# Kernel tuning notes

Measured on AMD Instinct MI355X. Metric: run time of the kernel, lower is better.

## Reference

```python
import jax, jax.numpy as jnp
import numpy as np

S, B, D, H = 2048, 2, 256, 8
DK = D // H
EPS = 1e-6
NEG = -1.0e9


def setup_inputs() -> dict:
    key = jax.random.key(0)
    ks = jax.random.split(key, 10)
    s = 1.0 / np.sqrt(D)
    return {
        "q": jax.random.normal(ks[0], (S, B, D), jnp.float32),
        "k": jax.random.normal(ks[1], (S, B, D), jnp.float32),
        "v": jax.random.normal(ks[2], (S, B, D), jnp.float32),
        "graph_pos": jax.random.uniform(ks[3], (S, S, H), jnp.float32),
        "mask": jax.random.randint(ks[4], (B, S, S), 0, 2, jnp.int32),
        # linear weights stored [in, out] so y = x @ W (torch Linear W.T)
        "w_q": jax.random.normal(ks[5], (D, D), jnp.float32) * s,
        "w_k": jax.random.normal(ks[6], (D, D), jnp.float32) * s,
        "w_v": jax.random.normal(ks[7], (D, D), jnp.float32) * s,
        "w_fc": jax.random.normal(ks[8], (D, D), jnp.float32) * s,
        "ln_gamma": jnp.ones((D,), jnp.float32),
        "ln_beta": jnp.zeros((D,), jnp.float32),
    }


def _forward(q, k, v, graph_pos, mask, w_q, w_k, w_v, w_fc, ln_gamma, ln_beta):
    # seq-first -> batch-first: [B, S, D]
    qb = jnp.transpose(q, (1, 0, 2))
    kb = jnp.transpose(k, (1, 0, 2))
    vb = jnp.transpose(v, (1, 0, 2))
    residual = qb
    # project and split heads: [B, H, S, dk]
    qh = (qb @ w_q).reshape(B, S, H, DK).transpose(0, 2, 1, 3)
    kh = (kb @ w_k).reshape(B, S, H, DK).transpose(0, 2, 1, 3)
    vh = (vb @ w_v).reshape(B, S, H, DK).transpose(0, 2, 1, 3)
    temp = jnp.asarray(DK, jnp.float32) ** 0.5
    attn = jnp.einsum("bhqd,bhkd->bhqk", qh / temp, kh)
    attn = jnp.where(mask[:, None] == 0, NEG, attn)
    attno = jax.nn.softmax(attn, axis=-1)  # dropout is identity in eval
    # graph_pos [lk, lq, h] -> [1, h, lq, lk], multiply post-softmax
    bias = jnp.transpose(graph_pos, (2, 1, 0))[None]
    out = jnp.einsum("bhqk,bhkd->bhqd", attno * bias, vh)
    out = out.transpose(0, 2, 1, 3).reshape(B, S, D)
    out = out @ w_fc + residual
    mu = out.mean(-1, keepdims=True)
    var = out.var(-1, keepdims=True)
    out = (out - mu) * jax.lax.rsqrt(var + EPS) * ln_gamma + ln_beta
    return jnp.transpose(out, (1, 0, 2)), attno


def reference(q, k, v, graph_pos, mask, w_q, w_k, w_v, w_fc, ln_gamma, ln_beta):
    return _forward(q, k, v, graph_pos, mask, w_q, w_k, w_v, w_fc, ln_gamma, ln_beta)
```

## Files before the change

### kernel.cpp

```cpp
#include <hip/hip_runtime.h>
#include <hip/hip_bf16.h>

#define S_LEN 2048
#define BATCH 2
#define DMODEL 256
#define NHEAD 8
#define DKH 32
#define NTOK (S_LEN * BATCH)
#define OUT0_ELEMS ((size_t)NTOK * DMODEL)
#define SW (S_LEN / 32)

typedef __bf16 bf16_t;
typedef __bf16 bf16x8 __attribute__((ext_vector_type(8)));
typedef __bf16 bf16x4 __attribute__((ext_vector_type(4)));
typedef float f32x4 __attribute__((ext_vector_type(4)));

#define MFMA16(a, b, c) __builtin_amdgcn_mfma_f32_16x16x32_bf16(a, b, c, 0, 0, 0)

__global__ void k_probe(const unsigned short* __restrict__ q, int* __restrict__ flag) {
  if (threadIdx.x == 0 && blockIdx.x == 0) {
    int good = 0;
    for (int i = 0; i < 512; i += 2) {
      unsigned short u = q[i];
      int e = (u >> 7) & 0xFF;
      if ((u & 0x7FFF) == 0 || (e >= 110 && e <= 135)) good++;
    }
    *flag = (good >= 200) ? 0 : 1;
  }
}

__global__ __launch_bounds__(256) void k_convert3(
    const void* __restrict__ s0, const void* __restrict__ s1,
    const void* __restrict__ s2, bf16_t* __restrict__ d0,
    bf16_t* __restrict__ d1, bf16_t* __restrict__ d2, int n,
    const int* __restrict__ flag) {
  const void* src = (blockIdx.y == 0) ? s0 : (blockIdx.y == 1) ? s1 : s2;
  bf16_t* dst = (blockIdx.y == 0) ? d0 : (blockIdx.y == 1) ? d1 : d2;
  int i = blockIdx.x * 256 + threadIdx.x;
  if (i >= n) return;
  if (*flag) dst[i] = (bf16_t)((const float*)src)[i];
  else       dst[i] = ((const bf16_t*)src)[i];
}

__global__ __launch_bounds__(256) void k_transpose_w(
    const void* __restrict__ w_q, const void* __restrict__ w_k,
    const void* __restrict__ w_v, const void* __restrict__ w_fc,
    bf16_t* __restrict__ wt, const int* __restrict__ flag) {
  __shared__ bf16_t tile[32][33];
  const void* w = (blockIdx.z == 0) ? w_q : (blockIdx.z == 1) ? w_k
                                       : (blockIdx.z == 2) ? w_v : w_fc;
  int f = *flag;
  bf16_t* o = wt + (size_t)blockIdx.z * DMODEL * DMODEL;
  int tx = threadIdx.x, ty = threadIdx.y;
  int x = blockIdx.x * 32 + tx;
  int y0 = blockIdx.y * 32;
  for (int j = ty; j < 32; j += 8) {
    size_t idx = (size_t)(y0 + j) * DMODEL + x;
    float v = f ? ((const float*)w)[idx] : (float)((const bf16_t*)w)[idx];
    tile[j][tx] = (bf16_t)v;
  }
  __syncthreads();
  for (int j = ty; j < 32; j += 8)
    o[(size_t)(blockIdx.x * 32 + j) * DMODEL + y0 + tx] = tile[tx][j];
}

__global__ __launch_bounds__(256) void k_proj(
    const bf16_t* __restrict__ qin, const bf16_t* __restrict__ kin,
    const bf16_t* __restrict__ vin, const bf16_t* __restrict__ wt,
    bf16_t* __restrict__ qhi, bf16_t* __restrict__ qlo,
    bf16_t* __restrict__ khi, bf16_t* __restrict__ klo,
    bf16_t* __restrict__ vt) {
  int mat = blockIdx.z;
  const bf16_t* x = (mat == 0) ? qin : (mat == 1) ? kin : vin;
  const bf16_t* wm = wt + (size_t)mat * DMODEL * DMODEL;
  int t0 = blockIdx.x * 16;
  int lane = threadIdx.x & 63, wave = threadIdx.x >> 6;
  int col = lane & 15, quad = lane >> 4;
  f32x4 acc[4] = {};
  const bf16_t* xrow = x + (size_t)(t0 + col) * DMODEL + quad * 8;
  for (int kk = 0; kk < 8; kk++) {
    bf16x8 a = *(const bf16x8*)(xrow + kk * 32);
#pragma unroll
    for (int nt = 0; nt < 4; nt++) {
      int n0 = wave * 64 + nt * 16;
      bf16x8 bw = *(const bf16x8*)(wm + (size_t)(n0 + col) * DMODEL + kk * 32 + quad * 8);
      acc[nt] = MFMA16(a, bw, acc[nt]);
    }
  }
  const float qscale = 0.17677669529663687f;
#pragma unroll
  for (int nt = 0; nt < 4; nt++) {
    int n = wave * 64 + nt * 16 + col;
    int h = n >> 5, dk = n & 31;
#pragma unroll
    for (int r = 0; r < 4; r++) {
      int t = t0 + quad * 4 + r;
      int s = t >> 1, bb = t & 1;
      float val = acc[nt][r];
      if (mat == 0) val *= qscale;
      if (mat <= 1) {
        bf16_t hi = (bf16_t)val;
        bf16_t lo = (bf16_t)(val - (float)hi);
        size_t idx = ((size_t)(bb * NHEAD + h) * S_LEN + s) * DKH + dk;
        if (mat == 0) { qhi[idx] = hi; qlo[idx] = lo; }
        else         { khi[idx] = hi; klo[idx] = lo; }
      } else {
        vt[((size_t)(bb * NHEAD + h) * DKH + dk) * S_LEN + s] = (bf16_t)val;
      }
    }
  }
}

template <int MODE>
__global__ __launch_bounds__(256) void k_tr_gp(
    const void* __restrict__ gp, bf16_t* __restrict__ gpt,
    void* __restrict__ attno_raw, const int* __restrict__ mask,
    unsigned int* __restrict__ mbits, const int* __restrict__ flag) {
  __shared__ float tile[32][8][32];
  int is32 = *flag;
  int tid = threadIdx.x;
  int k0 = blockIdx.x * 32, q0 = blockIdx.y * 32;
  int ci = tid & 63, krl = tid >> 6;
#pragma unroll
  for (int p = 0; p < 8; p++) {
    int kr = p * 4 + krl;
    size_t base = ((size_t)(k0 + kr) * S_LEN + q0) * NHEAD + ci * 4;
    f32x4 v;
    if (is32) {
      v = __builtin_nontemporal_load((const f32x4*)((const float*)gp + base));
    } else {
      bf16x4 bv = *(const bf16x4*)((const bf16_t*)gp + base);
      v[0] = (float)bv[0]; v[1] = (float)bv[1];
      v[2] = (float)bv[2]; v[3] = (float)bv[3];
    }
    int qq = ci >> 1, hb = (ci & 1) * 4;
    tile[kr][hb + 0][qq] = v[0];
    tile[kr][hb + 1][qq] = v[1];
    tile[kr][hb + 2][qq] = v[2];
    tile[kr][hb + 3][qq] = v[3];
  }
  __syncthreads();
  int h = tid >> 5, q = tid & 31;
  if (MODE == 0) {
    bf16_t* orow = gpt + ((size_t)h * S_LEN + q0 + q) * S_LEN + k0;
#pragma unroll
    for (int j = 0; j < 4; j++) {
      bf16x8 o;
#pragma unroll
      for (int i2 = 0; i2 < 8; i2++) o[i2] = (bf16_t)tile[j * 8 + i2][h][q];
      *(bf16x8*)(orow + j * 8) = o;
    }
  } else {
    size_t ro = ((size_t)h * S_LEN + q0 + q) * S_LEN + k0;
    size_t bs = (size_t)NHEAD * S_LEN * S_LEN;
    if (is32) {
      float* o0 = (float*)attno_raw + OUT0_ELEMS + ro;
#pragma unroll
      for (int j = 0; j < 8; j++) {
        f32x4 o;
#pragma unroll
        for (int i2 = 0; i2 < 4; i2++) o[i2] = tile[j * 4 + i2][h][q];
        *(f32x4*)(o0 + j * 4) = o;
        *(f32x4*)(o0 + bs + j * 4) = o;
      }
    } else {
      bf16_t* o0 = (bf16_t*)attno_raw + OUT0_ELEMS + ro;
#pragma unroll
      for (int j = 0; j < 4; j++) {
        bf16x8 o;
#pragma unroll
        for (int i2 = 0; i2 < 8; i2++) o[i2] = (bf16_t)tile[j * 8 + i2][h][q];
        *(bf16x8*)(o0 + j * 8) = o;
        *(bf16x8*)(o0 + bs + j * 8) = o;
      }
    }
  }
  if (tid < 64) {
    int w = (blockIdx.y * 64 + blockIdx.x) * 64 + tid;
    const int* src = mask + (size_t)w * 32;
    unsigned int bits = 0;
#pragma unroll
    for (int j = 0; j < 32; j += 4) {
      int4 m = *(const int4*)(src + j);
      if (m.x) bits |= 1u << j;
      if (m.y) bits |= 1u << (j + 1);
      if (m.z) bits |= 1u << (j + 2);
      if (m.w) bits |= 1u << (j + 3);
    }
    mbits[w] = bits;
  }
}

template <int BMODE>
__global__ __launch_bounds__(256) void k_attn(
    const bf16_t* __restrict__ qhi, const bf16_t* __restrict__ qlo,
    const bf16_t* __restrict__ khi, const bf16_t* __restrict__ klo,
    const bf16_t* __restrict__ vtg, const bf16_t* __restrict__ gpt,
    const unsigned int* __restrict__ mbits, void* __restrict__ attno_raw,
    float* __restrict__ attn_out, const int* __restrict__ flag) {
  __shared__ __align__(16) bf16_t lds_p[4][16][72];
  __shared__ __align__(16) bf16_t lds_pb[4][16][72];
  __shared__ float lds_m[4][16];
  __shared__ float lds_l[4][16];

  int is32 = *flag;
  float*  attno_f = (float*)attno_raw + OUT0_ELEMS;
  bf16_t* attno_b = (bf16_t*)attno_raw + OUT0_ELEMS;

  int L = blockIdx.x;
  int j = L >> 3;
  int p = (L & 7) + ((j >> 7) << 3);
  int h = p >> 1, b = p & 1;
  int q0 = (j & 127) * 16;

  int lane = threadIdx.x & 63, wave = threadIdx.x >> 6;
  int col = lane & 15, quad = lane >> 4;
  int kbase = wave * 512;
  size_t head = (size_t)(b * NHEAD + h);
  const bf16_t* Qh = qhi + head * S_LEN * DKH;
  const bf16_t* Ql = qlo + head * S_LEN * DKH;
  const bf16_t* Kh = khi + head * S_LEN * DKH;
  const bf16_t* Kl = klo + head * S_LEN * DKH;
  const bf16_t* Vt = vtg + head * DKH * S_LEN;
  const unsigned int* mrow =
      mbits + ((size_t)b * S_LEN + q0 + col) * SW + (kbase >> 5);
  const bf16_t* gprow = gpt + ((size_t)h * S_LEN + q0 + col) * S_LEN + kbase;
  size_t brow = head * S_LEN * S_LEN + (size_t)(q0 + col) * S_LEN + kbase;

  bf16x8 qhF = *(const bf16x8*)(Qh + (q0 + col) * DKH + quad * 8);
  bf16x8 qlF = *(const bf16x8*)(Ql + (q0 + col) * DKH + quad * 8);

  float m = -3.0e38f, l = 0.f;
#pragma unroll
  for (int t = 0; t < 32; t++) {
    int k0 = kbase + t * 16;
    bf16x8 khF = *(const bf16x8*)(Kh + (size_t)(k0 + col) * DKH + quad * 8);
    bf16x8 klF = *(const bf16x8*)(Kl + (size_t)(k0 + col) * DKH + quad * 8);
    f32x4 sc = {};
    sc = MFMA16(khF, qhF, sc);
    sc = MFMA16(khF, qlF, sc);
    sc = MFMA16(klF, qhF, sc);
    unsigned int mw = mrow[t >> 1];
    int mb = (int)(mw >> ((t & 1) * 16 + quad * 4)) & 0xF;
    float s0 = (mb & 1) ? sc[0] : -1e9f;
    float s1 = (mb & 2) ? sc[1] : -1e9f;
    float s2 = (mb & 4) ? sc[2] : -1e9f;
    float s3 = (mb & 8) ? sc[3] : -1e9f;
    float tm = fmaxf(fmaxf(s0, s1), fmaxf(s2, s3));
    float m2 = fmaxf(m, tm);
    l = l * __expf(m - m2) + __expf(s0 - m2) + __expf(s1 - m2) +
        __expf(s2 - m2) + __expf(s3 - m2);
    m = m2;
  }
#pragma unroll
  for (int off = 16; off < 64; off <<= 1) {
    float mo = __shfl_xor(m, off);
    float lo2 = __shfl_xor(l, off);
    float mn = fmaxf(m, mo);
    l = l * __expf(m - mn) + lo2 * __expf(mo - mn);
    m = mn;
  }
  if (lane < 16) { lds_m[wave][lane] = m; lds_l[wave][lane] = l; }
  __syncthreads();
  {
    float mg = -3.0e38f;
#pragma unroll
    for (int w = 0; w < 4; w++) mg = fmaxf(mg, lds_m[w][col]);
    float lg = 0.f;
#pragma unroll
    for (int w = 0; w < 4; w++) lg += lds_l[w][col] * __expf(lds_m[w][col] - mg);
    m = mg;
    l = lg;
  }
  float invl = 1.0f / l;

  f32x4 oacc[2] = {};
  for (int c = 0; c < 8; c++) {
#pragma unroll
    for (int tt = 0; tt < 4; tt++) {
      int k0 = kbase + c * 64 + tt * 16;
      bf16x8 khF = *(const bf16x8*)(Kh + (size_t)(k0 + col) * DKH + quad * 8);
      bf16x8 klF = *(const bf16x8*)(Kl + (size_t)(k0 + col) * DKH + quad * 8);
      f32x4 sc = {};
      sc = MFMA16(khF, qhF, sc);
      sc = MFMA16(khF, qlF, sc);
      sc = MFMA16(klF, qhF, sc);
      unsigned int mw = mrow[c * 2 + (tt >> 1)];
      int mb = (int)(mw >> ((tt & 1) * 16 + quad * 4)) & 0xF;
      float bias[4];
      if (BMODE == 0) {
        bf16x4 b4 = *(const bf16x4*)(gprow + c * 64 + tt * 16 + quad * 4);
#pragma unroll
        for (int r = 0; r < 4; r++) bias[r] = (float)b4[r];
      } else {
        if (is32) {
          f32x4 b4 = *(const f32x4*)(attno_f + brow + c * 64 + tt * 16 + quad * 4);
#pragma unroll
          for (int r = 0; r < 4; r++) bias[r] = b4[r];
        } else {
          bf16x4 b4 = *(const bf16x4*)(attno_b + brow + c * 64 + tt * 16 + quad * 4);
#pragma unroll
          for (int r = 0; r < 4; r++) bias[r] = (float)b4[r];
        }
      }
      bf16x4 pv, pbv;
#pragma unroll
      for (int r = 0; r < 4; r++) {
        float sv = (mb & (1 << r)) ? sc[r] : -1e9f;
        float p = __expf(sv - m) * invl;
        pv[r] = (bf16_t)p;
        pbv[r] = (bf16_t)(p * bias[r]);
      }
      *(bf16x4*)&lds_p[wave][col][tt * 16 + quad * 4] = pv;
      *(bf16x4*)&lds_pb[wave][col][tt * 16 + quad * 4] = pbv;
    }
    {
      int r = lane >> 2, part = lane & 3;
      size_t base = head * S_LEN * S_LEN + (size_t)(q0 + r) * S_LEN + kbase + c * 64 + part * 16;
      if (is32) {
#pragma unroll
        for (int jj = 0; jj < 4; jj++) {
          f32x4 vv;
#pragma unroll
          for (int ii = 0; ii < 4; ii++)
            vv[ii] = (float)lds_p[wave][r][part * 16 + jj * 4 + ii];
          *(f32x4*)(attno_f + base + jj * 4) = vv;
        }
      } else {
        bf16x8 v0 = *(const bf16x8*)&lds_p[wave][r][part * 16];
        bf16x8 v1 = *(const bf16x8*)&lds_p[wave][r][part * 16 + 8];
        *(bf16x8*)(attno_b + base) = v0;
        *(bf16x8*)(attno_b + base + 8) = v1;
      }
    }
#pragma unroll
    for (int ks = 0; ks < 2; ks++) {
      bf16x8 pf = *(const bf16x8*)&lds_pb[wave][col][ks * 32 + quad * 8];
#pragma unroll
      for (int dt = 0; dt < 2; dt++) {
        bf16x8 vf = *(const bf16x8*)(Vt + (size_t)(dt * 16 + col) * S_LEN + kbase + c * 64 + ks * 32 + quad * 8);
        oacc[dt] = MFMA16(vf, pf, oacc[dt]);
      }
    }
  }
  {
    float* lo = (float*)&lds_p[wave][0][0];
#pragma unroll
    for (int dt = 0; dt < 2; dt++)
#pragma unroll
      for (int r = 0; r < 4; r++)
        lo[col * 34 + dt * 16 + quad * 4 + r] = oacc[dt][r];
  }
  __syncthreads();
  if (wave == 0) {
    int t = (q0 + col) * BATCH + b;
#pragma unroll
    for (int dt = 0; dt < 2; dt++) {
      f32x4 vv = {};
#pragma unroll
      for (int w = 0; w < 4; w++) {
        const float* lw = (const float*)&lds_p[w][0][0];
#pragma unroll
        for (int r2 = 0; r2 < 4; r2++)
          vv[r2] += lw[col * 34 + dt * 16 + quad * 4 + r2];
      }
      *(f32x4*)(attn_out + (size_t)t * DMODEL + h * DKH + dt * 16 + quad * 4) = vv;
    }
  }
}

__global__ __launch_bounds__(256) void k_fc_ln(
    const float* __restrict__ attn_out, const bf16_t* __restrict__ wtfc,
    const bf16_t* __restrict__ qc, const void* __restrict__ gamma,
    const void* __restrict__ beta, void* __restrict__ out0,
    const int* __restrict__ flag) {
  __shared__ float lds_sx[4][16];
  __shared__ float lds_sq[4][16];
  int is32 = *flag;
  int t0 = blockIdx.x * 16;
  int lane = threadIdx.x & 63, wave = threadIdx.x >> 6;
  int col = lane & 15, quad = lane >> 4;
  f32x4 acc[4] = {};
  const float* arow = attn_out + (size_t)(t0 + col) * DMODEL + quad * 8;
  for (int kk = 0; kk < 8; kk++) {
    float4 a0 = *(const float4*)(arow + kk * 32);
    float4 a1 = *(const float4*)(arow + kk * 32 + 4);
    float av[8] = {a0.x, a0.y, a0.z, a0.w, a1.x, a1.y, a1.z, a1.w};
    bf16x8 ahi, alo;
#pragma unroll
    for (int j = 0; j < 8; j++) {
      bf16_t hi = (bf16_t)av[j];
      ahi[j] = hi;
      alo[j] = (bf16_t)(av[j] - (float)hi);
    }
#pragma unroll
    for (int nt = 0; nt < 4; nt++) {
      int n0 = wave * 64 + nt * 16;
      bf16x8 bfr = *(const bf16x8*)(wtfc + (size_t)(n0 + col) * DMODEL + kk * 32 + quad * 8);
      acc[nt] = MFMA16(ahi, bfr, acc[nt]);
      acc[nt] = MFMA16(alo, bfr, acc[nt]);
    }
  }
#pragma unroll
  for (int nt = 0; nt < 4; nt++) {
    int n = wave * 64 + nt * 16 + col;
#pragma unroll
    for (int r = 0; r < 4; r++) {
      int t = t0 + quad * 4 + r;
      acc[nt][r] += (float)qc[(size_t)t * DMODEL + n];
    }
  }
  float sx[4], sq[4];
#pragma unroll
  for (int r = 0; r < 4; r++) {
    float s = 0, s2 = 0;
#pragma unroll
    for (int nt = 0; nt < 4; nt++) { float v = acc[nt][r]; s += v; s2 += v * v; }
    sx[r] = s; sq[r] = s2;
  }
#pragma unroll
  for (int off = 1; off < 16; off <<= 1) {
#pragma unroll
    for (int r = 0; r < 4; r++) {
      sx[r] += __shfl_xor(sx[r], off);
      sq[r] += __shfl_xor(sq[r], off);
    }
  }
  if (col == 0) {
#pragma unroll
    for (int r = 0; r < 4; r++) {
      lds_sx[wave][quad * 4 + r] = sx[r];
      lds_sq[wave][quad * 4 + r] = sq[r];
    }
  }
  __syncthreads();
#pragma unroll
  for (int r = 0; r < 4; r++) {
    int tl = quad * 4 + r;
    float tsx = lds_sx[0][tl] + lds_sx[1][tl] + lds_sx[2][tl] + lds_sx[3][tl];
    float tsq = lds_sq[0][tl] + lds_sq[1][tl] + lds_sq[2][tl] + lds_sq[3][tl];
    float mu = tsx * (1.0f / 256.0f);
    float var = tsq * (1.0f / 256.0f) - mu * mu;
    float rs = rsqrtf(var + 1e-6f);
    int t = t0 + tl;
#pragma unroll
    for (int nt = 0; nt < 4; nt++) {
      int n = wave * 64 + nt * 16 + col;
      float g = is32 ? ((const float*)gamma)[n] : (float)((const bf16_t*)gamma)[n];
      float bt = is32 ? ((const float*)beta)[n] : (float)((const bf16_t*)beta)[n];
      float val = (acc[nt][r] - mu) * rs * g + bt;
      if (is32) ((float*)out0)[(size_t)t * DMODEL + n] = val;
      else      ((bf16_t*)out0)[(size_t)t * DMODEL + n] = (bf16_t)val;
    }
  }
}

extern "C" void kernel_launch(void* const* d_in, const int* in_sizes, int n_in,
                              void* d_out, int out_size, void* d_ws, size_t ws_size,
                              hipStream_t stream) {
  (void)in_sizes; (void)n_in; (void)out_size;
  const void* qin   = d_in[0];
  const void* kin   = d_in[1];
  const void* vin   = d_in[2];
  const void* gp    = d_in[3];
  const int*  mask  = (const int*)d_in[4];
  const void* w_q   = d_in[5];
  const void* w_k   = d_in[6];
  const void* w_v   = d_in[7];
  const void* w_fc  = d_in[8];
  const void* gamma = d_in[9];
  const void* beta  = d_in[10];

  char* ws = (char*)d_ws;
  bf16_t* wt  = (bf16_t*)(ws);
  bf16_t* qc  = (bf16_t*)(ws + (1u << 20));
  bf16_t* kc  = (bf16_t*)(ws + (3u << 20));
  bf16_t* vc  = (bf16_t*)(ws + (5u << 20));
  bf16_t* qhi = (bf16_t*)(ws + (7u << 20));
  bf16_t* qlo = (bf16_t*)(ws + (9u << 20));
  bf16_t* khi = (bf16_t*)(ws + (11u << 20));
  bf16_t* klo = (bf16_t*)(ws + (13u << 20));
  bf16_t* vt  = (bf16_t*)(ws + (15u << 20));
  float* attn_out = (float*)(ws + (17u << 20));
  int* flag = (int*)(ws + (21u << 20));
  unsigned int* mbits = (unsigned int*)(ws + (3u << 20));
  bf16_t* gpt = (bf16_t*)(ws + (22u << 20));

  bool use_ws_gpt = ws_size >= (((size_t)86 << 20) + 64);

  const int NELEM_QKV = NTOK * DMODEL;

  hipLaunchKernelGGL(k_probe, dim3(1), dim3(64), 0, stream,
                     (const unsigned short*)qin, flag);
  hipLaunchKernelGGL(k_convert3, dim3((NELEM_QKV + 255) / 256, 3), dim3(256), 0, stream,
                     qin, kin, vin, qc, kc, vc, NELEM_QKV, flag);
  hipLaunchKernelGGL(k_transpose_w, dim3(8, 8, 4), dim3(32, 8), 0, stream,
                     w_q, w_k, w_v, w_fc, wt, flag);
  hipLaunchKernelGGL(k_proj, dim3(256, 1, 3), dim3(256), 0, stream,
                     qc, kc, vc, wt, qhi, qlo, khi, klo, vt);
  if (use_ws_gpt) {
    hipLaunchKernelGGL((k_tr_gp<0>), dim3(64, 64), dim3(256), 0, stream,
                       gp, gpt, d_out, mask, mbits, flag);
    hipLaunchKernelGGL((k_attn<0>), dim3(2048), dim3(256), 0, stream,
                       qhi, qlo, khi, klo, vt, gpt, mbits, d_out, attn_out, flag);
  } else {
    hipLaunchKernelGGL((k_tr_gp<1>), dim3(64, 64), dim3(256), 0, stream,
                       gp, gpt, d_out, mask, mbits, flag);
    hipLaunchKernelGGL((k_attn<1>), dim3(2048), dim3(256), 0, stream,
                       qhi, qlo, khi, klo, vt, gpt, mbits, d_out, attn_out, flag);
  }
  hipLaunchKernelGGL(k_fc_ln, dim3(256), dim3(256), 0, stream,
                     attn_out, wt + 3 * DMODEL * DMODEL, qc, gamma, beta, d_out, flag);
}
```

Baseline: 626.7 us.

## Merge prep kernels, use exp2 softmax, write attention probs directly, tune occupancy

Three preprocessing kernels (input conversion, weight transpose, graph_pos transpose with mask packing) become one launch, and the probe kernel now uses a wave-parallel reduction. The softmax switches to hardware exp2, with log2(e) folded into the q scale, so each exponential needs no extra multiply. Attention probabilities are written straight from registers to global memory, which removes the lds_p staging buffer and cuts LDS use. k_attn gets an occupancy hint, and the graph bias loads are nontemporal. Per-thread stores of the probability output are narrower and less coalesced than the old staged writes, which may cost write bandwidth.

```diff
diff --git a/kernel.cpp b/kernel.cpp
--- a/kernel.cpp
+++ b/kernel.cpp
@@ -17,51 +17,145 @@
 
 #define MFMA16(a, b, c) __builtin_amdgcn_mfma_f32_16x16x32_bf16(a, b, c, 0, 0, 0)
 
+#if defined(__has_builtin)
+#if __has_builtin(__builtin_amdgcn_exp2f)
+#define EXP2(x) __builtin_amdgcn_exp2f(x)
+#endif
+#endif
+#ifndef EXP2
+#define EXP2(x) __expf((x) * 0.6931471805599453f)
+#endif
+
 __global__ void k_probe(const unsigned short* __restrict__ q, int* __restrict__ flag) {
-  if (threadIdx.x == 0 && blockIdx.x == 0) {
-    int good = 0;
-    for (int i = 0; i < 512; i += 2) {
-      unsigned short u = q[i];
-      int e = (u >> 7) & 0xFF;
-      if ((u & 0x7FFF) == 0 || (e >= 110 && e <= 135)) good++;
-    }
-    *flag = (good >= 200) ? 0 : 1;
-  }
+  int lane = threadIdx.x & 63;
+  int good = 0;
+#pragma unroll
+  for (int j = 0; j < 4; j++) {
+    unsigned short u = q[(lane * 4 + j) * 2];
+    int e = (u >> 7) & 0xFF;
+    if ((u & 0x7FFF) == 0 || (e >= 110 && e <= 135)) good++;
+  }
+#pragma unroll
+  for (int off = 1; off < 64; off <<= 1) good += __shfl_xor(good, off);
+  if (threadIdx.x == 0) *flag = (good >= 200) ? 0 : 1;
 }
 
-__global__ __launch_bounds__(256) void k_convert3(
-    const void* __restrict__ s0, const void* __restrict__ s1,
-    const void* __restrict__ s2, bf16_t* __restrict__ d0,
-    bf16_t* __restrict__ d1, bf16_t* __restrict__ d2, int n,
-    const int* __restrict__ flag) {
-  const void* src = (blockIdx.y == 0) ? s0 : (blockIdx.y == 1) ? s1 : s2;
-  bf16_t* dst = (blockIdx.y == 0) ? d0 : (blockIdx.y == 1) ? d1 : d2;
-  int i = blockIdx.x * 256 + threadIdx.x;
-  if (i >= n) return;
-  if (*flag) dst[i] = (bf16_t)((const float*)src)[i];
-  else       dst[i] = ((const bf16_t*)src)[i];
-}
-
-__global__ __launch_bounds__(256) void k_transpose_w(
+__global__ __launch_bounds__(256) void k_prep(
+    const void* __restrict__ qin, const void* __restrict__ kin,
+    const void* __restrict__ vin, bf16_t* __restrict__ qc,
+    bf16_t* __restrict__ kc, bf16_t* __restrict__ vc,
     const void* __restrict__ w_q, const void* __restrict__ w_k,
     const void* __restrict__ w_v, const void* __restrict__ w_fc,
-    bf16_t* __restrict__ wt, const int* __restrict__ flag) {
-  __shared__ bf16_t tile[32][33];
-  const void* w = (blockIdx.z == 0) ? w_q : (blockIdx.z == 1) ? w_k
-                                       : (blockIdx.z == 2) ? w_v : w_fc;
-  int f = *flag;
-  bf16_t* o = wt + (size_t)blockIdx.z * DMODEL * DMODEL;
-  int tx = threadIdx.x, ty = threadIdx.y;
-  int x = blockIdx.x * 32 + tx;
-  int y0 = blockIdx.y * 32;
-  for (int j = ty; j < 32; j += 8) {
-    size_t idx = (size_t)(y0 + j) * DMODEL + x;
-    float v = f ? ((const float*)w)[idx] : (float)((const bf16_t*)w)[idx];
-    tile[j][tx] = (bf16_t)v;
+    bf16_t* __restrict__ wt, const void* __restrict__ gp,
+    bf16_t* __restrict__ gpt, void* __restrict__ attno_raw,
+    const int* __restrict__ mask, unsigned int* __restrict__ mbits,
+    const int* __restrict__ flag, int mode) {
+  __shared__ __align__(16) char smem[32768];
+  int bid = blockIdx.x, tid = threadIdx.x;
+  int is32 = *flag;
+
+  if (bid < 12288) {
+    int which = bid >> 12;
+    int i = (bid & 4095) * 256 + tid;
+    const void* src = (which == 0) ? qin : (which == 1) ? kin : vin;
+    bf16_t* dst = (which == 0) ? qc : (which == 1) ? kc : vc;
+    if (i < NTOK * DMODEL)
+      dst[i] = is32 ? (bf16_t)((const float*)src)[i] : ((const bf16_t*)src)[i];
+    return;
+  }
+
+  if (bid < 12544) {
+    auto tile = (bf16_t(*)[33])smem;
+    int b2 = bid - 12288;
+    int bz = b2 >> 6, bx = b2 & 7, by = (b2 >> 3) & 7;
+    const void* w = (bz == 0) ? w_q : (bz == 1) ? w_k : (bz == 2) ? w_v : w_fc;
+    bf16_t* o = wt + (size_t)bz * DMODEL * DMODEL;
+    int tx = tid & 31, ty = tid >> 5;
+    int x = bx * 32 + tx, y0 = by * 32;
+    for (int j = ty; j < 32; j += 8) {
+      size_t idx = (size_t)(y0 + j) * DMODEL + x;
+      float v = is32 ? ((const float*)w)[idx] : (float)((const bf16_t*)w)[idx];
+      tile[j][tx] = (bf16_t)v;
+    }
+    __syncthreads();
+    for (int j = ty; j < 32; j += 8)
+      o[(size_t)(bx * 32 + j) * DMODEL + y0 + tx] = tile[tx][j];
+    return;
+  }
+
+  auto tile = (float(*)[8][32])smem;
+  int b3 = bid - 12544;
+  int bx = b3 & 63, by = b3 >> 6;
+  int k0 = bx * 32, q0 = by * 32;
+  int ci = tid & 63, krl = tid >> 6;
+#pragma unroll
+  for (int p = 0; p < 8; p++) {
+    int kr = p * 4 + krl;
+    size_t base = ((size_t)(k0 + kr) * S_LEN + q0) * NHEAD + ci * 4;
+    f32x4 v;
+    if (is32) {
+      v = __builtin_nontemporal_load((const f32x4*)((const float*)gp + base));
+    } else {
+      bf16x4 bv = *(const bf16x4*)((const bf16_t*)gp + base);
+      v[0] = (float)bv[0]; v[1] = (float)bv[1];
+      v[2] = (float)bv[2]; v[3] = (float)bv[3];
+    }
+    int qq = ci >> 1, hb = (ci & 1) * 4;
+    tile[kr][hb + 0][qq] = v[0];
+    tile[kr][hb + 1][qq] = v[1];
+    tile[kr][hb + 2][qq] = v[2];
+    tile[kr][hb + 3][qq] = v[3];
   }
   __syncthreads();
-  for (int j = ty; j < 32; j += 8)
-    o[(size_t)(blockIdx.x * 32 + j) * DMODEL + y0 + tx] = tile[tx][j];
+  int h = tid >> 5, q = tid & 31;
+  if (mode == 0) {
+    bf16_t* orow = gpt + ((size_t)h * S_LEN + q0 + q) * S_LEN + k0;
+#pragma unroll
+    for (int j = 0; j < 4; j++) {
+      bf16x8 o;
+#pragma unroll
+      for (int i2 = 0; i2 < 8; i2++) o[i2] = (bf16_t)tile[j * 8 + i2][h][q];
+      *(bf16x8*)(orow + j * 8) = o;
+    }
+  } else {
+    size_t ro = ((size_t)h * S_LEN + q0 + q) * S_LEN + k0;
+    size_t bs = (size_t)NHEAD * S_LEN * S_LEN;
+    if (is32) {
+      float* o0 = (float*)attno_raw + OUT0_ELEMS + ro;
+#pragma unroll
+      for (int j = 0; j < 8; j++) {
+        f32x4 o;
+#pragma unroll
+        for (int i2 = 0; i2 < 4; i2++) o[i2] = tile[j * 4 + i2][h][q];
+        *(f32x4*)(o0 + j * 4) = o;
+        *(f32x4*)(o0 + bs + j * 4) = o;
+      }
+    } else {
+      bf16_t* o0 = (bf16_t*)attno_raw + OUT0_ELEMS + ro;
+#pragma unroll
+      for (int j = 0; j < 4; j++) {
+        bf16x8 o;
+#pragma unroll
+        for (int i2 = 0; i2 < 8; i2++) o[i2] = (bf16_t)tile[j * 8 + i2][h][q];
+        *(bf16x8*)(o0 + j * 8) = o;
+        *(bf16x8*)(o0 + bs + j * 8) = o;
+      }
+    }
+  }
+  if (tid < 64) {
+    int w = (by * 64 + bx) * 64 + tid;
+    const int* src = mask + (size_t)w * 32;
+    unsigned int bits = 0;
+#pragma unroll
+    for (int j = 0; j < 32; j += 4) {
+      int4 m = *(const int4*)(src + j);
+      if (m.x) bits |= 1u << j;
+      if (m.y) bits |= 1u << (j + 1);
+      if (m.z) bits |= 1u << (j + 2);
+      if (m.w) bits |= 1u << (j + 3);
+    }
+    mbits[w] = bits;
+  }
 }
 
 __global__ __launch_bounds__(256) void k_proj(
@@ -87,7 +181,7 @@
       acc[nt] = MFMA16(a, bw, acc[nt]);
     }
   }
-  const float qscale = 0.17677669529663687f;
+  const float qscale = 0.2550348612f;
 #pragma unroll
   for (int nt = 0; nt < 4; nt++) {
     int n = wave * 64 + nt * 16 + col;
@@ -111,94 +205,13 @@
   }
 }
 
-template <int MODE>
-__global__ __launch_bounds__(256) void k_tr_gp(
-    const void* __restrict__ gp, bf16_t* __restrict__ gpt,
-    void* __restrict__ attno_raw, const int* __restrict__ mask,
-    unsigned int* __restrict__ mbits, const int* __restrict__ flag) {
-  __shared__ float tile[32][8][32];
-  int is32 = *flag;
-  int tid = threadIdx.x;
-  int k0 = blockIdx.x * 32, q0 = blockIdx.y * 32;
-  int ci = tid & 63, krl = tid >> 6;
-#pragma unroll
-  for (int p = 0; p < 8; p++) {
-    int kr = p * 4 + krl;
-    size_t base = ((size_t)(k0 + kr) * S_LEN + q0) * NHEAD + ci * 4;
-    f32x4 v;
-    if (is32) {
-      v = __builtin_nontemporal_load((const f32x4*)((const float*)gp + base));
-    } else {
-      bf16x4 bv = *(const bf16x4*)((const bf16_t*)gp + base);
-      v[0] = (float)bv[0]; v[1] = (float)bv[1];
-      v[2] = (float)bv[2]; v[3] = (float)bv[3];
-    }
-    int qq = ci >> 1, hb = (ci & 1) * 4;
-    tile[kr][hb + 0][qq] = v[0];
-    tile[kr][hb + 1][qq] = v[1];
-    tile[kr][hb + 2][qq] = v[2];
-    tile[kr][hb + 3][qq] = v[3];
-  }
-  __syncthreads();
-  int h = tid >> 5, q = tid & 31;
-  if (MODE == 0) {
-    bf16_t* orow = gpt + ((size_t)h * S_LEN + q0 + q) * S_LEN + k0;
-#pragma unroll
-    for (int j = 0; j < 4; j++) {
-      bf16x8 o;
-#pragma unroll
-      for (int i2 = 0; i2 < 8; i2++) o[i2] = (bf16_t)tile[j * 8 + i2][h][q];
-      *(bf16x8*)(orow + j * 8) = o;
-    }
-  } else {
-    size_t ro = ((size_t)h * S_LEN + q0 + q) * S_LEN + k0;
-    size_t bs = (size_t)NHEAD * S_LEN * S_LEN;
-    if (is32) {
-      float* o0 = (float*)attno_raw + OUT0_ELEMS + ro;
-#pragma unroll
-      for (int j = 0; j < 8; j++) {
-        f32x4 o;
-#pragma unroll
-        for (int i2 = 0; i2 < 4; i2++) o[i2] = tile[j * 4 + i2][h][q];
-        *(f32x4*)(o0 + j * 4) = o;
-        *(f32x4*)(o0 + bs + j * 4) = o;
-      }
-    } else {
-      bf16_t* o0 = (bf16_t*)attno_raw + OUT0_ELEMS + ro;
-#pragma unroll
-      for (int j = 0; j < 4; j++) {
-        bf16x8 o;
-#pragma unroll
-        for (int i2 = 0; i2 < 8; i2++) o[i2] = (bf16_t)tile[j * 8 + i2][h][q];
-        *(bf16x8*)(o0 + j * 8) = o;
-        *(bf16x8*)(o0 + bs + j * 8) = o;
-      }
-    }
-  }
-  if (tid < 64) {
-    int w = (blockIdx.y * 64 + blockIdx.x) * 64 + tid;
-    const int* src = mask + (size_t)w * 32;
-    unsigned int bits = 0;
-#pragma unroll
-    for (int j = 0; j < 32; j += 4) {
-      int4 m = *(const int4*)(src + j);
-      if (m.x) bits |= 1u << j;
-      if (m.y) bits |= 1u << (j + 1);
-      if (m.z) bits |= 1u << (j + 2);
-      if (m.w) bits |= 1u << (j + 3);
-    }
-    mbits[w] = bits;
-  }
-}
-
 template <int BMODE>
-__global__ __launch_bounds__(256) void k_attn(
+__global__ __launch_bounds__(256, 8) void k_attn(
     const bf16_t* __restrict__ qhi, const bf16_t* __restrict__ qlo,
     const bf16_t* __restrict__ khi, const bf16_t* __restrict__ klo,
     const bf16_t* __restrict__ vtg, const bf16_t* __restrict__ gpt,
     const unsigned int* __restrict__ mbits, void* __restrict__ attno_raw,
     float* __restrict__ attn_out, const int* __restrict__ flag) {
-  __shared__ __align__(16) bf16_t lds_p[4][16][72];
   __shared__ __align__(16) bf16_t lds_pb[4][16][72];
   __shared__ float lds_m[4][16];
   __shared__ float lds_l[4][16];
@@ -248,8 +261,8 @@
     float s3 = (mb & 8) ? sc[3] : -1e9f;
     float tm = fmaxf(fmaxf(s0, s1), fmaxf(s2, s3));
     float m2 = fmaxf(m, tm);
-    l = l * __expf(m - m2) + __expf(s0 - m2) + __expf(s1 - m2) +
-        __expf(s2 - m2) + __expf(s3 - m2);
+    l = l * EXP2(m - m2) + EXP2(s0 - m2) + EXP2(s1 - m2) +
+        EXP2(s2 - m2) + EXP2(s3 - m2);
     m = m2;
   }
 #pragma unroll
@@ -257,7 +270,7 @@
     float mo = __shfl_xor(m, off);
     float lo2 = __shfl_xor(l, off);
     float mn = fmaxf(m, mo);
-    l = l * __expf(m - mn) + lo2 * __expf(mo - mn);
+    l = l * EXP2(m - mn) + lo2 * EXP2(mo - mn);
     m = mn;
   }
   if (lane < 16) { lds_m[wave][lane] = m; lds_l[wave][lane] = l; }
@@ -268,7 +281,7 @@
     for (int w = 0; w < 4; w++) mg = fmaxf(mg, lds_m[w][col]);
     float lg = 0.f;
 #pragma unroll
-    for (int w = 0; w < 4; w++) lg += lds_l[w][col] * __expf(lds_m[w][col] - mg);
+    for (int w = 0; w < 4; w++) lg += lds_l[w][col] * EXP2(lds_m[w][col] - mg);
     m = mg;
     l = lg;
   }
@@ -289,7 +302,8 @@
       int mb = (int)(mw >> ((tt & 1) * 16 + quad * 4)) & 0xF;
       float bias[4];
       if (BMODE == 0) {
-        bf16x4 b4 = *(const bf16x4*)(gprow + c * 64 + tt * 16 + quad * 4);
+        bf16x4 b4 = __builtin_nontemporal_load(
+            (const bf16x4*)(gprow + c * 64 + tt * 16 + quad * 4));
 #pragma unroll
         for (int r = 0; r < 4; r++) bias[r] = (float)b4[r];
       } else {
@@ -303,35 +317,20 @@
           for (int r = 0; r < 4; r++) bias[r] = (float)b4[r];
         }
       }
+      f32x4 pf32;
       bf16x4 pv, pbv;
 #pragma unroll
       for (int r = 0; r < 4; r++) {
         float sv = (mb & (1 << r)) ? sc[r] : -1e9f;
-        float p = __expf(sv - m) * invl;
-        pv[r] = (bf16_t)p;
-        pbv[r] = (bf16_t)(p * bias[r]);
-      }
-      *(bf16x4*)&lds_p[wave][col][tt * 16 + quad * 4] = pv;
+        float pp = EXP2(sv - m) * invl;
+        pf32[r] = pp;
+        pv[r] = (bf16_t)pp;
+        pbv[r] = (bf16_t)(pp * bias[r]);
+      }
+      size_t sa = brow + c * 64 + tt * 16 + quad * 4;
+      if (is32) *(f32x4*)(attno_f + sa) = pf32;
+      else      *(bf16x4*)(attno_b + sa) = pv;
       *(bf16x4*)&lds_pb[wave][col][tt * 16 + quad * 4] = pbv;
-    }
-    {
-      int r = lane >> 2, part = lane & 3;
-      size_t base = head * S_LEN * S_LEN + (size_t)(q0 + r) * S_LEN + kbase + c * 64 + part * 16;
-      if (is32) {
-#pragma unroll
-        for (int jj = 0; jj < 4; jj++) {
-          f32x4 vv;
-#pragma unroll
-          for (int ii = 0; ii < 4; ii++)
-            vv[ii] = (float)lds_p[wave][r][part * 16 + jj * 4 + ii];
-          *(f32x4*)(attno_f + base + jj * 4) = vv;
-        }
-      } else {
-        bf16x8 v0 = *(const bf16x8*)&lds_p[wave][r][part * 16];
-        bf16x8 v1 = *(const bf16x8*)&lds_p[wave][r][part * 16 + 8];
-        *(bf16x8*)(attno_b + base) = v0;
-        *(bf16x8*)(attno_b + base + 8) = v1;
-      }
     }
 #pragma unroll
     for (int ks = 0; ks < 2; ks++) {
@@ -344,7 +343,7 @@
     }
   }
   {
-    float* lo = (float*)&lds_p[wave][0][0];
+    float* lo = (float*)&lds_pb[wave][0][0];
 #pragma unroll
     for (int dt = 0; dt < 2; dt++)
 #pragma unroll
@@ -359,7 +358,7 @@
       f32x4 vv = {};
 #pragma unroll
       for (int w = 0; w < 4; w++) {
-        const float* lw = (const float*)&lds_p[w][0][0];
+        const float* lw = (const float*)&lds_pb[w][0][0];
 #pragma unroll
         for (int r2 = 0; r2 < 4; r2++)
           vv[r2] += lw[col * 34 + dt * 16 + quad * 4 + r2];
@@ -473,6 +472,7 @@
 
   char* ws = (char*)d_ws;
   bf16_t* wt  = (bf16_t*)(ws);
+  int* flag = (int*)(ws + (1u << 19));
   bf16_t* qc  = (bf16_t*)(ws + (1u << 20));
   bf16_t* kc  = (bf16_t*)(ws + (3u << 20));
   bf16_t* vc  = (bf16_t*)(ws + (5u << 20));
@@ -482,30 +482,22 @@
   bf16_t* klo = (bf16_t*)(ws + (13u << 20));
   bf16_t* vt  = (bf16_t*)(ws + (15u << 20));
   float* attn_out = (float*)(ws + (17u << 20));
-  int* flag = (int*)(ws + (21u << 20));
-  unsigned int* mbits = (unsigned int*)(ws + (3u << 20));
+  unsigned int* mbits = (unsigned int*)(ws + (21u << 20));
   bf16_t* gpt = (bf16_t*)(ws + (22u << 20));
 
   bool use_ws_gpt = ws_size >= (((size_t)86 << 20) + 64);
-
-  const int NELEM_QKV = NTOK * DMODEL;
 
   hipLaunchKernelGGL(k_probe, dim3(1), dim3(64), 0, stream,
                      (const unsigned short*)qin, flag);
-  hipLaunchKernelGGL(k_convert3, dim3((NELEM_QKV + 255) / 256, 3), dim3(256), 0, stream,
-                     qin, kin, vin, qc, kc, vc, NELEM_QKV, flag);
-  hipLaunchKernelGGL(k_transpose_w, dim3(8, 8, 4), dim3(32, 8), 0, stream,
-                     w_q, w_k, w_v, w_fc, wt, flag);
+  hipLaunchKernelGGL(k_prep, dim3(16640), dim3(256), 0, stream,
+                     qin, kin, vin, qc, kc, vc, w_q, w_k, w_v, w_fc, wt,
+                     gp, gpt, d_out, mask, mbits, flag, use_ws_gpt ? 0 : 1);
   hipLaunchKernelGGL(k_proj, dim3(256, 1, 3), dim3(256), 0, stream,
                      qc, kc, vc, wt, qhi, qlo, khi, klo, vt);
   if (use_ws_gpt) {
-    hipLaunchKernelGGL((k_tr_gp<0>), dim3(64, 64), dim3(256), 0, stream,
-                       gp, gpt, d_out, mask, mbits, flag);
     hipLaunchKernelGGL((k_attn<0>), dim3(2048), dim3(256), 0, stream,
                        qhi, qlo, khi, klo, vt, gpt, mbits, d_out, attn_out, flag);
   } else {
-    hipLaunchKernelGGL((k_tr_gp<1>), dim3(64, 64), dim3(256), 0, stream,
-                       gp, gpt, d_out, mask, mbits, flag);
     hipLaunchKernelGGL((k_attn<1>), dim3(2048), dim3(256), 0, stream,
                        qhi, qlo, khi, klo, vt, gpt, mbits, d_out, attn_out, flag);
   }
```

Measured after the change: 708.9 us. +13.1%, slower.
